# Kernel tuning notes

Hardware: AMD Instinct MI355X
Metric: run time of the kernel (lower is better)

The kernel has to match this reference:

```python
import jax, jax.numpy as jnp
import numpy as np

K = 5          # kernel_size
BETA = 15.0    # soft-max temperature
PAD = (K - 1) // 2  # fixed_padding with dilation=1: pad_beg = pad_end = 2


def setup_inputs() -> dict:
    key = jax.random.key(0)
    kx, kw = jax.random.split(key)
    x = jax.random.normal(kx, (16, 8, 256, 256), dtype=jnp.float32)
    weight = jax.random.normal(kw, (8, 8, K, K), dtype=jnp.float32) * 0.1
    return {"x": x, "weight": weight}


def reference(x, weight):
    """Morphological dilation2d with soft-max (logsumexp) reduction.

    Equivalent to: unfold(pad(x)) -> (B,1,C*K*K,L); add weight.view(O,-1);
    logsumexp(beta * .) / beta over the C*K*K axis; reshape to (B,O,H,W).
    Implemented as a streaming logsumexp over the K*K taps to avoid the
    huge unfold intermediate.
    """
    B, C, H, W = x.shape
    O = weight.shape[0]
    xp = jnp.pad(x, ((0, 0), (0, 0), (PAD, PAD), (PAD, PAD)))
    acc = None
    for ki in range(K):
        for kj in range(K):
            xs = xp[:, :, ki:ki + H, kj:kj + W]              # (B,C,H,W)
            w_tap = weight[:, :, ki, kj]                      # (O,C)
            # beta * (w + x), broadcast to (B,O,C,H,W)
            t = BETA * (xs[:, None, :, :, :] + w_tap[None, :, :, None, None])
            lse = jax.nn.logsumexp(t, axis=2)                 # (B,O,H,W)
            acc = lse if acc is None else jnp.logaddexp(acc, lse)
    return acc / BETA
```

## Files before the change

kernel.cpp:

```cpp
#include <hip/hip_runtime.h>
#include <hip/hip_bf16.h>
#include <math.h>

#define KW 5
#define BETA 15.0f
#define MSHIFT 3.0f
#define CIN 8
#define COUT 8
#define HH 256
#define WW 256
#define TWW 16
#define TWH 8
#define WCW 20
#define WCH 12
#define WSLOTS (WCW * WCH)

typedef float f32x4 __attribute__((ext_vector_type(4)));
typedef short s16x8 __attribute__((ext_vector_type(8)));

static __device__ __forceinline__ unsigned f2bf(float f) {
    unsigned u = __float_as_uint(f);
    return (u + 0x7FFFu + ((u >> 16) & 1u)) >> 16;
}

__global__ void build_afrag(const float* __restrict__ wgt,
                            s16x8* __restrict__ table) {
    int i = blockIdx.x * 64 + threadIdx.x;
    if (i >= 7 * 64) return;
    int g = i >> 6, lane = i & 63;
    int quad = lane >> 4, row = lane & 15;
    int tap = g * 4 + quad;
    s16x8 af;
    #pragma unroll
    for (int j = 0; j < CIN; ++j) {
        float v = 0.0f;
        if (tap < 25 && row < COUT)
            v = __expf(BETA * wgt[(row * CIN + j) * (KW * KW) + tap]);
        af[j] = (short)f2bf(v);
    }
    table[i] = af;
}

__global__ __launch_bounds__(256, 6) void morph_mfma(
    const float* __restrict__ x, const s16x8* __restrict__ table,
    float* __restrict__ out)
{
    __shared__ int4 exs[4 * WSLOTS];

    const int tid  = threadIdx.x;
    const int lane = tid & 63;
    const int wv   = tid >> 6;
    const int px   = lane & 15;
    const int quad = lane >> 4;

    const int lid = blockIdx.x;
    const int sw  = (lid & 7) * 256 + (lid >> 3);
    const int b   = sw >> 7;
    const int t   = sw & 127;
    const int h0  = (t >> 2) * TWH;
    const int w0  = (t & 3) * 64 + wv * TWW;

    int4* myex = &exs[wv * WSLOTS];

    s16x8 afrag[7];
    int   toff[7];
    #pragma unroll
    for (int g = 0; g < 7; ++g) {
        afrag[g] = table[g * 64 + lane];
        int tap = g * 4 + quad;
        int tc  = tap < 25 ? tap : 24;
        toff[g] = (tc / KW) * WCW + (tc % KW);
    }

    for (int s = lane; s < WSLOTS; s += 64) {
        int r = s / WCW, col = s - r * WCW;
        int gh = h0 + r - 2, gw = w0 + col - 2;
        bool ok = ((unsigned)gh < (unsigned)HH) & ((unsigned)gw < (unsigned)WW);
        unsigned pk[4];
        #pragma unroll
        for (int c2 = 0; c2 < 4; ++c2) {
            float v0 = 0.0f, v1 = 0.0f;
            if (ok) {
                v0 = x[((b * CIN + 2 * c2) * HH + gh) * WW + gw];
                v1 = x[((b * CIN + 2 * c2 + 1) * HH + gh) * WW + gw];
            }
            float2 e = make_float2(__expf(BETA * (v0 - MSHIFT)),
                                   __expf(BETA * (v1 - MSHIFT)));
            __hip_bfloat162 h2 = __float22bfloat162_rn(e);
            pk[c2] = *reinterpret_cast<unsigned*>(&h2);
        }
        int4 p; p.x = pk[0]; p.y = pk[1]; p.z = pk[2]; p.w = pk[3];
        myex[s] = p;
    }

    const float inv_beta = 1.0f / BETA;
    #pragma unroll
    for (int hl = 0; hl < TWH; ++hl) {
        const int base = hl * WCW + px;
        f32x4 acc0 = {0.0f, 0.0f, 0.0f, 0.0f};
        f32x4 acc1 = {0.0f, 0.0f, 0.0f, 0.0f};
        #pragma unroll
        for (int g = 0; g < 7; ++g) {
            s16x8 bfr = *(const s16x8*)&myex[base + toff[g]];
            if (g & 1)
                acc1 = __builtin_amdgcn_mfma_f32_16x16x32_bf16(
                           afrag[g], bfr, acc1, 0, 0, 0);
            else
                acc0 = __builtin_amdgcn_mfma_f32_16x16x32_bf16(
                           afrag[g], bfr, acc0, 0, 0, 0);
        }
        if (quad < 2) {
            #pragma unroll
            for (int r = 0; r < 4; ++r) {
                int o = quad * 4 + r;
                out[((b * COUT + o) * HH + h0 + hl) * WW + w0 + px]
                    = MSHIFT + __logf(acc0[r] + acc1[r]) * inv_beta;
            }
        }
    }
}

extern "C" void kernel_launch(void* const* d_in, const int* in_sizes, int n_in,
                              void* d_out, int out_size, void* d_ws, size_t ws_size,
                              hipStream_t stream) {
    const float* x   = (const float*)d_in[0];
    const float* wgt = (const float*)d_in[1];
    float* out  = (float*)d_out;
    s16x8* tab  = (s16x8*)d_ws;

    const int B = in_sizes[0] / (CIN * HH * WW);
    const int nblk = B * (HH / TWH) * (WW / 64);
    build_afrag<<<7, 64, 0, stream>>>(wgt, tab);
    morph_mfma<<<nblk, 256, 0, stream>>>(x, tab, out);
}
```

Baseline: 98.61 us.

## Pack two output rows into each MFMA using shifted weight rows

The A-fragment table now stores the 8 output channels for row h in rows 0-7 and, in rows 8-15, the same weights shifted down by one tap row, so they produce output row h+1. Taps grow to 30, handled as 8 groups. One pass of 8 MFMAs thus yields two output rows and fills all 16 MFMA output rows, where before 7 MFMAs yielded one row with half the rows unused. The exp and log calls are also replaced by native exp2/log2 with folded constants, and the launch-bounds occupancy hint drops from 6 to 5.

New measurement: 94.89 us. -3.8%, faster.

```diff
diff --git a/kernel.cpp b/kernel.cpp
--- a/kernel.cpp
+++ b/kernel.cpp
@@ -14,6 +14,7 @@
 #define WCW 20
 #define WCH 12
 #define WSLOTS (WCW * WCH)
+#define NG 8
 
 typedef float f32x4 __attribute__((ext_vector_type(4)));
 typedef short s16x8 __attribute__((ext_vector_type(8)));
@@ -26,22 +27,29 @@
 __global__ void build_afrag(const float* __restrict__ wgt,
                             s16x8* __restrict__ table) {
     int i = blockIdx.x * 64 + threadIdx.x;
-    if (i >= 7 * 64) return;
     int g = i >> 6, lane = i & 63;
     int quad = lane >> 4, row = lane & 15;
-    int tap = g * 4 + quad;
+    int tap30 = g * 4 + quad;
+    int tr = tap30 / KW, tc = tap30 % KW;
     s16x8 af;
     #pragma unroll
     for (int j = 0; j < CIN; ++j) {
         float v = 0.0f;
-        if (tap < 25 && row < COUT)
-            v = __expf(BETA * wgt[(row * CIN + j) * (KW * KW) + tap]);
+        if (tap30 < 30) {
+            if (row < COUT) {
+                if (tr <= 4)
+                    v = __expf(BETA * wgt[(row * CIN + j) * (KW * KW) + tr * KW + tc]);
+            } else {
+                if (tr >= 1)
+                    v = __expf(BETA * wgt[((row - 8) * CIN + j) * (KW * KW) + (tr - 1) * KW + tc]);
+            }
+        }
         af[j] = (short)f2bf(v);
     }
     table[i] = af;
 }
 
-__global__ __launch_bounds__(256, 6) void morph_mfma(
+__global__ __launch_bounds__(256, 5) void morph_mfma(
     const float* __restrict__ x, const s16x8* __restrict__ table,
     float* __restrict__ out)
 {
@@ -62,14 +70,14 @@
 
     int4* myex = &exs[wv * WSLOTS];
 
-    s16x8 afrag[7];
-    int   toff[7];
+    s16x8 afrag[NG];
+    int   toff[NG];
     #pragma unroll
-    for (int g = 0; g < 7; ++g) {
+    for (int g = 0; g < NG; ++g) {
         afrag[g] = table[g * 64 + lane];
-        int tap = g * 4 + quad;
-        int tc  = tap < 25 ? tap : 24;
-        toff[g] = (tc / KW) * WCW + (tc % KW);
+        int tap30 = g * 4 + quad;
+        int tcl   = tap30 < 30 ? tap30 : 29;
+        toff[g] = (tcl / KW) * WCW + (tcl % KW);
     }
 
     for (int s = lane; s < WSLOTS; s += 64) {
@@ -84,8 +92,9 @@
                 v0 = x[((b * CIN + 2 * c2) * HH + gh) * WW + gw];
                 v1 = x[((b * CIN + 2 * c2 + 1) * HH + gh) * WW + gw];
             }
-            float2 e = make_float2(__expf(BETA * (v0 - MSHIFT)),
-                                   __expf(BETA * (v1 - MSHIFT)));
+            float2 e = make_float2(
+                __builtin_amdgcn_exp2f(fmaf(v0, 21.6404256f, -64.9212768f)),
+                __builtin_amdgcn_exp2f(fmaf(v1, 21.6404256f, -64.9212768f)));
             __hip_bfloat162 h2 = __float22bfloat162_rn(e);
             pk[c2] = *reinterpret_cast<unsigned*>(&h2);
         }
@@ -93,14 +102,16 @@
         myex[s] = p;
     }
 
-    const float inv_beta = 1.0f / BETA;
+    const int dh = quad >> 1;
+    const int ob = (quad & 1) * 4;
+    const float LN2B = 0.04620981f;
     #pragma unroll
-    for (int hl = 0; hl < TWH; ++hl) {
-        const int base = hl * WCW + px;
+    for (int hp = 0; hp < 4; ++hp) {
+        const int base = (2 * hp) * WCW + px;
         f32x4 acc0 = {0.0f, 0.0f, 0.0f, 0.0f};
         f32x4 acc1 = {0.0f, 0.0f, 0.0f, 0.0f};
         #pragma unroll
-        for (int g = 0; g < 7; ++g) {
+        for (int g = 0; g < NG; ++g) {
             s16x8 bfr = *(const s16x8*)&myex[base + toff[g]];
             if (g & 1)
                 acc1 = __builtin_amdgcn_mfma_f32_16x16x32_bf16(
@@ -109,13 +120,12 @@
                 acc0 = __builtin_amdgcn_mfma_f32_16x16x32_bf16(
                            afrag[g], bfr, acc0, 0, 0, 0);
         }
-        if (quad < 2) {
-            #pragma unroll
-            for (int r = 0; r < 4; ++r) {
-                int o = quad * 4 + r;
-                out[((b * COUT + o) * HH + h0 + hl) * WW + w0 + px]
-                    = MSHIFT + __logf(acc0[r] + acc1[r]) * inv_beta;
-            }
+        const int h = h0 + 2 * hp + dh;
+        #pragma unroll
+        for (int r = 0; r < 4; ++r) {
+            float s = acc0[r] + acc1[r];
+            out[((b * COUT + ob + r) * HH + h) * WW + w0 + px]
+                = fmaf(__builtin_amdgcn_logf(s), LN2B, MSHIFT);
         }
     }
 }
@@ -130,6 +140,6 @@
 
     const int B = in_sizes[0] / (CIN * HH * WW);
     const int nblk = B * (HH / TWH) * (WW / 64);
-    build_afrag<<<7, 64, 0, stream>>>(wgt, tab);
+    build_afrag<<<NG, 64, 0, stream>>>(wgt, tab);
     morph_mfma<<<nblk, 256, 0, stream>>>(x, tab, out);
 }
```
